# Kernel tuning notes

Measured on AMD Instinct MI355X. Metric: run time of the kernel, lower is better.

The kernel has to match this reference:

```python
import jax, jax.numpy as jnp
import numpy as np

B, S, D, K, ITERS = 16, 4096, 1024, 16, 3
SCALE = D ** -0.5
EPS_LN = 1e-5
EPS_ATTN = 1e-8


def setup_inputs() -> dict:
    key = jax.random.key(0)
    ks = jax.random.split(key, 16)

    def lin_w(k, out_d, in_d):
        return (jax.random.uniform(k, (out_d, in_d)) * 2 - 1) / np.sqrt(in_d)

    return {
        "tokens": jax.random.normal(ks[0], (B, S, D), dtype=jnp.float32),
        "slot_mu": jax.random.normal(ks[1], (1, K, D), dtype=jnp.float32) * 0.02,
        "Wq": lin_w(ks[2], D, D), "bq": jnp.zeros((D,), jnp.float32),
        "Wk": lin_w(ks[3], D, D), "bk": jnp.zeros((D,), jnp.float32),
        "Wv": lin_w(ks[4], D, D), "bv": jnp.zeros((D,), jnp.float32),
        "W_ih": lin_w(ks[5], 3 * D, D), "b_ih": jnp.zeros((3 * D,), jnp.float32),
        "W_hh": lin_w(ks[6], 3 * D, D), "b_hh": jnp.zeros((3 * D,), jnp.float32),
        "W1": lin_w(ks[7], 4 * D, D), "b1": jnp.zeros((4 * D,), jnp.float32),
        "W2": lin_w(ks[8], D, 4 * D), "b2": jnp.zeros((D,), jnp.float32),
        "g_slots": jnp.ones((D,), jnp.float32), "b_slots": jnp.zeros((D,), jnp.float32),
        "g_mlp": jnp.ones((D,), jnp.float32), "b_mlp": jnp.zeros((D,), jnp.float32),
    }


def _ln(x, g, b):
    mu = jnp.mean(x, axis=-1, keepdims=True)
    var = jnp.mean(jnp.square(x - mu), axis=-1, keepdims=True)
    return (x - mu) * jax.lax.rsqrt(var + EPS_LN) * g + b


def reference(tokens, slot_mu, Wq, bq, Wk, bk, Wv, bv,
              W_ih, b_ih, W_hh, b_hh, W1, b1, W2, b2,
              g_slots, b_slots, g_mlp, b_mlp):
    # eval-mode slot init: slots = mu (no reparameterization noise)
    slots = jnp.broadcast_to(slot_mu, (tokens.shape[0], K, D))
    k = tokens @ Wk.T + bk  # (B,S,D)
    v = tokens @ Wv.T + bv  # (B,S,D)
    attn = None
    for _ in range(ITERS):
        slots_prev = slots
        q = _ln(slots, g_slots, b_slots) @ Wq.T + bq            # (B,K,D)
        logits = jnp.einsum('bkd,bsd->bks', q, k) * SCALE        # (B,K,S)
        attn = jax.nn.softmax(logits, axis=1)                    # softmax over slots K
        attn_n = attn / (jnp.sum(attn, axis=2, keepdims=True) + EPS_ATTN)
        updates = jnp.einsum('bks,bsd->bkd', attn_n, v)          # (B,K,D)
        # GRUCell(updates, slots_prev)
        gi = updates @ W_ih.T + b_ih                             # (B,K,3D)
        gh = slots_prev @ W_hh.T + b_hh
        ir, iz, in_ = jnp.split(gi, 3, axis=-1)
        hr, hz, hn = jnp.split(gh, 3, axis=-1)
        r = jax.nn.sigmoid(ir + hr)
        z = jax.nn.sigmoid(iz + hz)
        n = jnp.tanh(in_ + r * hn)
        slots = (1.0 - z) * n + z * slots_prev
        # MLP residual
        h = _ln(slots, g_mlp, b_mlp)
        slots = slots + jax.nn.gelu(h @ W1.T + b1, approximate=False) @ W2.T + b2
    return slots, attn
```

## Files before the change

### kernel.cpp

```cpp
#include <hip/hip_runtime.h>


typedef unsigned short u16;
typedef unsigned int u32;
typedef float f32x4 __attribute__((ext_vector_type(4)));
typedef unsigned int u32x4 __attribute__((ext_vector_type(4)));
typedef __bf16 bf16x8 __attribute__((ext_vector_type(8)));

#define B_ 16
#define S_ 4096
#define D_ 1024
#define K_ 16
#define SCALE_ 0.03125f

__device__ __forceinline__ float b2f(u16 u) {
  u32 x = ((u32)u) << 16;
  return __builtin_bit_cast(float, x);
}
__device__ __forceinline__ u16 f2b(float f) {
  u32 u = __builtin_bit_cast(u32, f);
  u32 r = (u + 0x7fffu + ((u >> 16) & 1u)) >> 16;
  return (u16)r;
}
__device__ __forceinline__ bf16x8 ld16g(const u16* p) {
  return __builtin_bit_cast(bf16x8, *(const u32x4*)p);
}
__device__ __forceinline__ void gload_lds16(const void* g, void* l) {
  __builtin_amdgcn_global_load_lds(
      (const __attribute__((address_space(1))) void*)g,
      (__attribute__((address_space(3))) void*)l, 16, 0, 0);
}

__global__ void convert8_kernel(const float* __restrict__ src,
                                u16* __restrict__ dst, int n8) {
  const int idx = blockIdx.x * 256 + threadIdx.x;
  if (idx >= n8) return;
  const float* s = src + (size_t)idx * 8;
  const f32x4 lo = *(const f32x4*)s;
  const f32x4 hi = *(const f32x4*)(s + 4);
  union { u16 h[8]; u32x4 q; } u;
#pragma unroll
  for (int j = 0; j < 4; ++j) { u.h[j] = f2b(lo[j]); u.h[4 + j] = f2b(hi[j]); }
  *(u32x4*)(dst + (size_t)idx * 8) = u.q;
}

__global__ __launch_bounds__(256) void transcvt_kernel(
    const float* __restrict__ src, u16* __restrict__ dst, int R, int C) {
  const int r0 = blockIdx.x * 64;
  const int c0 = blockIdx.y * 64;
  const int cl = threadIdx.x & 63;
  const int rq = threadIdx.x >> 6;
#pragma unroll
  for (int h = 0; h < 2; ++h) {
    const int rbase = (rq + h * 4) * 8;
    union { u16 u[8]; u32x4 q; } w;
#pragma unroll
    for (int j = 0; j < 8; ++j)
      w.u[j] = f2b(src[(size_t)(r0 + rbase + j) * C + c0 + cl]);
    *(u32x4*)&dst[(size_t)(c0 + cl) * R + r0 + rbase] = w.q;
  }
}

__global__ void colvec_kernel(const float* __restrict__ W,
                              const float* __restrict__ x,
                              float* __restrict__ out, int R, int C) {
  const int c = blockIdx.x * 256 + threadIdx.x;
  const int r0 = blockIdx.y * 64;
  if (c >= C) return;
  float acc = 0.f;
#pragma unroll 8
  for (int r = 0; r < 64; ++r)
    acc = fmaf(W[(size_t)(r0 + r) * C + c], x[r0 + r], acc);
  atomicAdd(&out[c], acc);
}

__global__ __launch_bounds__(256) void rowvec_kernel(
    const float* __restrict__ W, const float* __restrict__ x,
    const float* __restrict__ add, float* __restrict__ out, int R, int C) {
  const int wave = threadIdx.x >> 6, lane = threadIdx.x & 63;
  const int r = blockIdx.x * 4 + wave;
  if (r >= R) return;
  float acc = 0.f;
  for (int c = lane; c < C; c += 64) acc = fmaf(W[(size_t)r * C + c], x[c], acc);
#pragma unroll
  for (int off = 1; off < 64; off <<= 1) acc += __shfl_xor(acc, off);
  if (lane == 0) out[r] = add[r] + acc;
}

__global__ __launch_bounds__(256) void qdot_kernel(
    const u16* __restrict__ lnq, const float* __restrict__ qdw,
    const float* __restrict__ bq, const float* __restrict__ bk,
    float* __restrict__ out) {
  const int wave = threadIdx.x >> 6, lane = threadIdx.x & 63;
  const int m = blockIdx.x * 4 + wave;
  float acc = 0.f;
  for (int a = lane; a < D_; a += 64)
    acc = fmaf(b2f(lnq[(size_t)m * D_ + a]), qdw[a], acc);
  for (int d = lane; d < D_; d += 64) acc = fmaf(bq[d], bk[d], acc);
#pragma unroll
  for (int off = 1; off < 64; off <<= 1) acc += __shfl_xor(acc, off);
  if (lane == 0) out[m] = acc;
}

__global__ __launch_bounds__(256) void gemm128_bb(
    const u16* __restrict__ A, const u16* __restrict__ Bw,
    const float* __restrict__ bias, u16* __restrict__ C, int N, int Kd,
    int mtiles) {
  __shared__ __align__(16) u16 At[128 * 64];
  __shared__ __align__(16) u16 Bt[128 * 64];
  const int tid = threadIdx.x;
  const int ntiles = N >> 7;
  const int nwg = mtiles * ntiles;
  const int cpx = nwg >> 3;
  const int lin = blockIdx.x;
  const int wg = (lin & 7) * cpx + (lin >> 3);
  const int m0 = (wg / ntiles) * 128;
  const int n0 = (wg % ntiles) * 128;
  const int wave = tid >> 6, lane = tid & 63;
  const int q4 = lane >> 4, l16 = lane & 15;
  const int wm = (wave & 1) * 64, wn = (wave >> 1) * 64;

  f32x4 acc[4][4];
#pragma unroll
  for (int i = 0; i < 4; ++i)
#pragma unroll
    for (int j = 0; j < 4; ++j) acc[i][j] = 0.f;

  const int trow = tid >> 3;
  const int tcol = ((tid & 7) * 8) ^ ((trow & 7) << 3);
  const u16* ga = A + (size_t)(m0 + trow) * Kd + tcol;
  const u16* gb = Bw + (size_t)(n0 + trow) * Kd + tcol;
  u16* la = At + tid * 8;
  u16* lb = Bt + tid * 8;

  for (int k0 = 0; k0 < Kd; k0 += 64) {
    __syncthreads();
#pragma unroll
    for (int c = 0; c < 4; ++c)
      gload_lds16(ga + (size_t)c * 32 * Kd + k0, la + c * 2048);
#pragma unroll
    for (int c = 0; c < 4; ++c)
      gload_lds16(gb + (size_t)c * 32 * Kd + k0, lb + c * 2048);
    __syncthreads();
#pragma unroll
    for (int kk = 0; kk < 64; kk += 32) {
      bf16x8 af[4], bfr[4];
#pragma unroll
      for (int i = 0; i < 4; ++i) {
        const int row = wm + i * 16 + l16;
        const int byo = row * 128 + ((kk * 2 + q4 * 16) ^ ((row & 7) << 4));
        af[i] = *(const bf16x8*)((const char*)At + byo);
      }
#pragma unroll
      for (int j = 0; j < 4; ++j) {
        const int row = wn + j * 16 + l16;
        const int byo = row * 128 + ((kk * 2 + q4 * 16) ^ ((row & 7) << 4));
        bfr[j] = *(const bf16x8*)((const char*)Bt + byo);
      }
#pragma unroll
      for (int i = 0; i < 4; ++i)
#pragma unroll
        for (int j = 0; j < 4; ++j)
          acc[i][j] = __builtin_amdgcn_mfma_f32_16x16x32_bf16(af[i], bfr[j],
                                                              acc[i][j], 0, 0, 0);
    }
  }
#pragma unroll
  for (int j = 0; j < 4; ++j) {
    const int col = n0 + wn + j * 16 + l16;
    const float bv = bias ? bias[col] : 0.f;
#pragma unroll
    for (int i = 0; i < 4; ++i) {
      const int rowb = m0 + wm + i * 16 + q4 * 4;
#pragma unroll
      for (int r = 0; r < 4; ++r)
        C[(size_t)(rowb + r) * N + col] = f2b(acc[i][j][r] + bv);
    }
  }
}

template <int MODE>
__global__ __launch_bounds__(256) void gemm64_bt(
    const u16* __restrict__ A, const u16* __restrict__ Bw,
    const float* __restrict__ bias, float* Cf, u16* Cb, const float* resid,
    int N, int Kd) {
  __shared__ __align__(16) u16 At[64 * 64];
  __shared__ __align__(16) u16 Bt[64 * 64];
  const int tid = threadIdx.x;
  const int m0 = blockIdx.x * 64;
  const int n0 = blockIdx.y * 64;
  const int wave = tid >> 6, lane = tid & 63;
  const int q4 = lane >> 4, l16 = lane & 15;
  const int wm = (wave & 1) * 32, wn = (wave >> 1) * 32;

  f32x4 acc[2][2];
#pragma unroll
  for (int i = 0; i < 2; ++i)
#pragma unroll
    for (int j = 0; j < 2; ++j) acc[i][j] = 0.f;

  const int r_ = tid >> 3;
  const int c8 = (tid & 7) * 8;
  const int c8s = c8 ^ ((r_ & 7) << 3);

  for (int k0 = 0; k0 < Kd; k0 += 64) {
    u32x4 ta[2], tb[2];
#pragma unroll
    for (int i = 0; i < 2; ++i) {
      ta[i] = *(const u32x4*)(A + (size_t)(m0 + r_ + i * 32) * Kd + k0 + c8);
      tb[i] = *(const u32x4*)(Bw + (size_t)(n0 + r_ + i * 32) * Kd + k0 + c8);
    }
    __syncthreads();
#pragma unroll
    for (int i = 0; i < 2; ++i) {
      *(u32x4*)&At[(r_ + i * 32) * 64 + c8s] = ta[i];
      *(u32x4*)&Bt[(r_ + i * 32) * 64 + c8s] = tb[i];
    }
    __syncthreads();
#pragma unroll
    for (int kk = 0; kk < 64; kk += 32) {
      bf16x8 af[2], bfr[2];
#pragma unroll
      for (int i = 0; i < 2; ++i) {
        const int row = wm + i * 16 + l16;
        const int byo = row * 128 + ((kk * 2 + q4 * 16) ^ ((row & 7) << 4));
        af[i] = *(const bf16x8*)((const char*)At + byo);
      }
#pragma unroll
      for (int j = 0; j < 2; ++j) {
        const int row = wn + j * 16 + l16;
        const int byo = row * 128 + ((kk * 2 + q4 * 16) ^ ((row & 7) << 4));
        bfr[j] = *(const bf16x8*)((const char*)Bt + byo);
      }
#pragma unroll
      for (int i = 0; i < 2; ++i)
#pragma unroll
        for (int j = 0; j < 2; ++j)
          acc[i][j] = __builtin_amdgcn_mfma_f32_16x16x32_bf16(af[i], bfr[j],
                                                              acc[i][j], 0, 0, 0);
    }
  }
#pragma unroll
  for (int j = 0; j < 2; ++j) {
    const int col = n0 + wn + j * 16 + l16;
    const float bv = bias[col];
#pragma unroll
    for (int i = 0; i < 2; ++i) {
      const int rowb = m0 + wm + i * 16 + q4 * 4;
#pragma unroll
      for (int r = 0; r < 4; ++r) {
        const int row = rowb + r;
        float val = acc[i][j][r] + bv;
        if constexpr (MODE == 0) {
          Cb[(size_t)row * N + col] = f2b(val);
        } else if constexpr (MODE == 1) {
          Cf[(size_t)row * N + col] = val;
        } else if constexpr (MODE == 2) {
          val = 0.5f * val * (1.f + erff(val * 0.70710678118654752f));
          Cb[(size_t)row * N + col] = f2b(val);
        } else {
          const float rv = resid[(size_t)row * N + col];
          Cf[(size_t)row * N + col] = val + rv;
        }
      }
    }
  }
}

__global__ __launch_bounds__(256) void attn_pass1(
    const u16* __restrict__ qb, const u16* __restrict__ tok,
    const float* __restrict__ qdot, float* __restrict__ attn_t,
    float* __restrict__ rowsum, float* __restrict__ attn_out) {
  const int b = blockIdx.y;
  const int wave = threadIdx.x >> 6, lane = threadIdx.x & 63;
  const int q4 = lane >> 4, l16 = lane & 15;
  const int tok0 = blockIdx.x * 256 + wave * 64;
  const u16* ap = qb + (size_t)(b * 16 + l16) * D_ + q4 * 8;
  const u16* bp = tok + ((size_t)b * S_ + tok0 + l16) * D_ + q4 * 8;
  const f32x4 qd = *(const f32x4*)&qdot[b * 16 + q4 * 4];
  f32x4 acc[4];
#pragma unroll
  for (int j = 0; j < 4; ++j) acc[j] = 0.f;
  for (int k0 = 0; k0 < D_; k0 += 32) {
    bf16x8 a = ld16g(ap + k0);
#pragma unroll
    for (int j = 0; j < 4; ++j) {
      bf16x8 bb = ld16g(bp + (size_t)j * 16 * D_ + k0);
      acc[j] = __builtin_amdgcn_mfma_f32_16x16x32_bf16(a, bb, acc[j], 0, 0, 0);
    }
  }
  float rs[4] = {0.f, 0.f, 0.f, 0.f};
#pragma unroll
  for (int j = 0; j < 4; ++j) {
    const int token = tok0 + j * 16 + l16;
    float l[4];
#pragma unroll
    for (int r = 0; r < 4; ++r) l[r] = acc[j][r] * SCALE_ + qd[r];
    float mx = fmaxf(fmaxf(l[0], l[1]), fmaxf(l[2], l[3]));
    mx = fmaxf(mx, __shfl_xor(mx, 16));
    mx = fmaxf(mx, __shfl_xor(mx, 32));
    float e[4], ssum = 0.f;
#pragma unroll
    for (int r = 0; r < 4; ++r) { e[r] = __expf(l[r] - mx); ssum += e[r]; }
    ssum += __shfl_xor(ssum, 16);
    ssum += __shfl_xor(ssum, 32);
    const float inv = 1.f / ssum;
    f32x4 p;
#pragma unroll
    for (int r = 0; r < 4; ++r) { p[r] = e[r] * inv; rs[r] += p[r]; }
    *(f32x4*)(attn_t + ((size_t)b * S_ + token) * 16 + q4 * 4) = p;
    if (attn_out) {
#pragma unroll
      for (int r = 0; r < 4; ++r)
        attn_out[(size_t)(b * 16 + q4 * 4 + r) * S_ + token] = p[r];
    }
  }
#pragma unroll
  for (int r = 0; r < 4; ++r) {
    float v = rs[r];
    v += __shfl_xor(v, 1);
    v += __shfl_xor(v, 2);
    v += __shfl_xor(v, 4);
    v += __shfl_xor(v, 8);
    if (l16 == 0) atomicAdd(&rowsum[b * 16 + q4 * 4 + r], v);
  }
}

__global__ __launch_bounds__(256) void attn_pass2(
    const float* __restrict__ attn_t, const u16* __restrict__ tok,
    float* __restrict__ uprime) {
  const int b = blockIdx.y;
  const int dchunk = blockIdx.x & 1;
  const int ssplit = blockIdx.x >> 1;
  const int d = dchunk * 512 + threadIdx.x * 2;
  const int s0 = ssplit * 512;
  const u16* vp = tok + ((size_t)b * S_ + s0) * D_ + d;
  const float* ap = attn_t + ((size_t)b * S_ + s0) * 16;
  float acc0[16], acc1[16];
#pragma unroll
  for (int k = 0; k < 16; ++k) { acc0[k] = 0.f; acc1[k] = 0.f; }
#pragma unroll 4
  for (int s = 0; s < 512; ++s) {
    const u32 vv2 = *(const u32*)(vp + (size_t)s * D_);
    const float v0 = b2f((u16)(vv2 & 0xffffu));
    const float v1 = b2f((u16)(vv2 >> 16));
    const float* ar = ap + s * 16;
#pragma unroll
    for (int k = 0; k < 16; ++k) {
      const float a = ar[k];
      acc0[k] = fmaf(a, v0, acc0[k]);
      acc1[k] = fmaf(a, v1, acc1[k]);
    }
  }
#pragma unroll
  for (int k = 0; k < 16; ++k) {
    atomicAdd(&uprime[(size_t)(b * 16 + k) * D_ + d], acc0[k]);
    atomicAdd(&uprime[(size_t)(b * 16 + k) * D_ + d + 1], acc1[k]);
  }
}

__global__ void normcvt_kernel(const float* __restrict__ updates,
                               const float* __restrict__ rowsum,
                               u16* __restrict__ out) {
  const int idx = blockIdx.x * 256 + threadIdx.x;
  const int m = idx >> 10;
  const float inv = 1.f / (rowsum[m] + 1e-8f);
  out[idx] = f2b(updates[idx] * inv);
}

__global__ __launch_bounds__(256) void ln_kernel(
    const float* __restrict__ x, const float* __restrict__ g,
    const float* __restrict__ bb, u16* __restrict__ out_ln,
    u16* __restrict__ out_raw) {
  const int row = blockIdx.x, tid = threadIdx.x;
  const float* xr = x + (size_t)row * D_;
  float v[4], s = 0.f, ss = 0.f;
#pragma unroll
  for (int i = 0; i < 4; ++i) {
    v[i] = xr[tid + i * 256];
    s += v[i];
    ss += v[i] * v[i];
  }
#pragma unroll
  for (int off = 1; off < 64; off <<= 1) {
    s += __shfl_xor(s, off);
    ss += __shfl_xor(ss, off);
  }
  __shared__ float sh[8];
  if ((tid & 63) == 0) { sh[tid >> 6] = s; sh[4 + (tid >> 6)] = ss; }
  __syncthreads();
  s = sh[0] + sh[1] + sh[2] + sh[3];
  ss = sh[4] + sh[5] + sh[6] + sh[7];
  const float mu = s * (1.f / 1024.f);
  float var = ss * (1.f / 1024.f) - mu * mu;
  var = fmaxf(var, 0.f);
  const float rstd = rsqrtf(var + 1e-5f);
#pragma unroll
  for (int i = 0; i < 4; ++i) {
    const int dd = tid + i * 256;
    out_ln[(size_t)row * D_ + dd] =
        f2b((v[i] - mu) * rstd * g[dd] + bb[dd]);
    if (out_raw) out_raw[(size_t)row * D_ + dd] = f2b(v[i]);
  }
}

__global__ void gru_kernel(const float* __restrict__ gi,
                           const float* __restrict__ gh,
                           float* __restrict__ slots) {
  const int idx = blockIdx.x * 256 + threadIdx.x;
  const int m = idx >> 10, dd = idx & 1023;
  const size_t base = (size_t)m * 3072 + dd;
  const float ir = gi[base], iz = gi[base + 1024], in_ = gi[base + 2048];
  const float hr = gh[base], hz = gh[base + 1024], hn = gh[base + 2048];
  const float r = 1.f / (1.f + __expf(-(ir + hr)));
  const float z = 1.f / (1.f + __expf(-(iz + hz)));
  const float n = tanhf(in_ + r * hn);
  slots[idx] = (1.f - z) * n + z * slots[idx];
}

__global__ void init_slots_kernel(const float* __restrict__ mu,
                                  float* __restrict__ slots) {
  const int idx = blockIdx.x * 256 + threadIdx.x;
  slots[idx] = mu[idx & (K_ * D_ - 1)];
}

__global__ void store_slots_kernel(const float* __restrict__ slots,
                                   float* __restrict__ out) {
  const int idx = blockIdx.x * 256 + threadIdx.x;
  out[idx] = slots[idx];
}

extern "C" void kernel_launch(void* const* d_in, const int* in_sizes, int n_in,
                              void* d_out, int out_size, void* d_ws,
                              size_t ws_size, hipStream_t stream) {
  const float* tokens = (const float*)d_in[0];
  const float* slot_mu = (const float*)d_in[1];
  const float* Wq = (const float*)d_in[2];
  const float* bq = (const float*)d_in[3];
  const float* Wk = (const float*)d_in[4];
  const float* bk = (const float*)d_in[5];
  const float* Wv = (const float*)d_in[6];
  const float* bv = (const float*)d_in[7];
  const float* W_ih = (const float*)d_in[8];
  const float* b_ih = (const float*)d_in[9];
  const float* W_hh = (const float*)d_in[10];
  const float* b_hh = (const float*)d_in[11];
  const float* W1 = (const float*)d_in[12];
  const float* b1 = (const float*)d_in[13];
  const float* W2 = (const float*)d_in[14];
  const float* b2 = (const float*)d_in[15];
  const float* g_slots = (const float*)d_in[16];
  const float* b_slots = (const float*)d_in[17];
  const float* g_mlp = (const float*)d_in[18];
  const float* b_mlp = (const float*)d_in[19];

  char* p = (char*)d_ws;
  auto alloc = [&](size_t bytes) {
    char* r = p;
    p += (bytes + 255) & ~(size_t)255;
    return r;
  };
  u16* tokb = (u16*)alloc((size_t)B_ * S_ * D_ * 2);
  float* attn_t = (float*)alloc((size_t)B_ * S_ * K_ * 4);
  float* slots = (float*)alloc((size_t)B_ * K_ * D_ * 4);
  float* updates = (float*)alloc((size_t)B_ * K_ * D_ * 4);
  float* rowsum = (float*)alloc(1024);
  float* gi = (float*)alloc((size_t)B_ * K_ * 3 * D_ * 4);
  float* gh = (float*)alloc((size_t)B_ * K_ * 3 * D_ * 4);
  u16* slots_bf16 = (u16*)alloc((size_t)B_ * K_ * D_ * 2);
  u16* slots_ln_bf16 = (u16*)alloc((size_t)B_ * K_ * D_ * 2);
  u16* qkbuf = (u16*)alloc((size_t)B_ * K_ * D_ * 2);
  u16* updates_bf16 = (u16*)alloc((size_t)B_ * K_ * D_ * 2);
  u16* h_bf16 = (u16*)alloc((size_t)B_ * K_ * D_ * 2);
  u16* act_bf16 = (u16*)alloc((size_t)B_ * K_ * 4 * D_ * 2);
  float* qdotbuf = (float*)alloc(256 * 4);
  float* qd_w = (float*)alloc(D_ * 4);
  float* qkbias = (float*)alloc(D_ * 4);
  float* bihv = (float*)alloc(3 * D_ * 4);
  u16* cWih = (u16*)alloc((size_t)3 * D_ * D_ * 2);
  u16* cWhh = (u16*)alloc((size_t)3 * D_ * D_ * 2);
  u16* cW1 = (u16*)alloc((size_t)4 * D_ * D_ * 2);
  u16* cW2 = (u16*)alloc((size_t)4 * D_ * D_ * 2);
  u16* cWqT = (u16*)alloc((size_t)D_ * D_ * 2);
  u16* cWkT = (u16*)alloc((size_t)D_ * D_ * 2);
  u16* cWvT = (u16*)alloc((size_t)D_ * D_ * 2);
  u16* cPT = (u16*)alloc((size_t)D_ * D_ * 2);
  u16* cWihv = (u16*)alloc((size_t)3 * D_ * D_ * 2);
  if ((size_t)(p - (char*)d_ws) > ws_size) return;

  float* out_slots = (float*)d_out;
  float* out_attn = (float*)d_out + (size_t)B_ * K_ * D_;

  convert8_kernel<<<(3 * D_ * D_ / 8 + 255) / 256, 256, 0, stream>>>(W_ih, cWih, 3 * D_ * D_ / 8);
  convert8_kernel<<<(3 * D_ * D_ / 8 + 255) / 256, 256, 0, stream>>>(W_hh, cWhh, 3 * D_ * D_ / 8);
  convert8_kernel<<<(4 * D_ * D_ / 8 + 255) / 256, 256, 0, stream>>>(W1, cW1, 4 * D_ * D_ / 8);
  convert8_kernel<<<(4 * D_ * D_ / 8 + 255) / 256, 256, 0, stream>>>(W2, cW2, 4 * D_ * D_ / 8);
  convert8_kernel<<<(B_ * S_ * D_ / 8 + 255) / 256, 256, 0, stream>>>(
      tokens, tokb, B_ * S_ * D_ / 8);
  transcvt_kernel<<<dim3(16, 16), 256, 0, stream>>>(Wq, cWqT, D_, D_);
  transcvt_kernel<<<dim3(16, 16), 256, 0, stream>>>(Wk, cWkT, D_, D_);
  transcvt_kernel<<<dim3(16, 16), 256, 0, stream>>>(Wv, cWvT, D_, D_);

  gemm128_bb<<<64, 256, 0, stream>>>(cWkT, cWqT, nullptr, cPT, D_, D_, 8);
  gemm128_bb<<<192, 256, 0, stream>>>(cWih, cWvT, nullptr, cWihv, D_, D_, 24);

  hipMemsetAsync(qkbias, 0, D_ * 4, stream);
  hipMemsetAsync(qd_w, 0, D_ * 4, stream);
  colvec_kernel<<<dim3(4, 16), 256, 0, stream>>>(Wk, bq, qkbias, D_, D_);
  colvec_kernel<<<dim3(4, 16), 256, 0, stream>>>(Wq, bk, qd_w, D_, D_);
  rowvec_kernel<<<768, 256, 0, stream>>>(W_ih, bv, b_ih, bihv, 3 * D_, D_);

  init_slots_kernel<<<1024, 256, 0, stream>>>(slot_mu, slots);

  for (int it = 0; it < 3; ++it) {
    ln_kernel<<<256, 256, 0, stream>>>(slots, g_slots, b_slots, slots_ln_bf16,
                                       slots_bf16);
    gemm64_bt<0><<<dim3(4, 16), 256, 0, stream>>>(slots_ln_bf16, cPT, qkbias,
                                                  nullptr, qkbuf, nullptr, D_, D_);
    qdot_kernel<<<64, 256, 0, stream>>>(slots_ln_bf16, qd_w, bq, bk, qdotbuf);
    hipMemsetAsync(updates, 0, (size_t)B_ * K_ * D_ * 4 + 1024, stream);
    attn_pass1<<<dim3(16, 16), 256, 0, stream>>>(
        qkbuf, tokb, qdotbuf, attn_t, rowsum, (it == 2) ? out_attn : nullptr);
    attn_pass2<<<dim3(16, 16), 256, 0, stream>>>(attn_t, tokb, updates);
    normcvt_kernel<<<1024, 256, 0, stream>>>(updates, rowsum, updates_bf16);
    gemm64_bt<1><<<dim3(4, 48), 256, 0, stream>>>(updates_bf16, cWihv, bihv, gi,
                                                  nullptr, nullptr, 3 * D_, D_);
    gemm64_bt<1><<<dim3(4, 48), 256, 0, stream>>>(slots_bf16, cWhh, b_hh, gh,
                                                  nullptr, nullptr, 3 * D_, D_);
    gru_kernel<<<1024, 256, 0, stream>>>(gi, gh, slots);
    ln_kernel<<<256, 256, 0, stream>>>(slots, g_mlp, b_mlp, h_bf16, nullptr);
    gemm64_bt<2><<<dim3(4, 64), 256, 0, stream>>>(h_bf16, cW1, b1, nullptr,
                                                  act_bf16, nullptr, 4 * D_, D_);
    gemm64_bt<3><<<dim3(4, 16), 256, 0, stream>>>(act_bf16, cW2, b2, slots,
                                                  nullptr, slots, D_, 4 * D_);
  }
  store_slots_kernel<<<1024, 256, 0, stream>>>(slots, out_slots);
}
```

Baseline: 1.191 ms.

## Fuse attention passes and fold qdot, GRU, LN and memset kernels

Merges the logits/softmax pass and the attention-weighted value reduction into one kernel. Softmax probabilities now stay in LDS, so the fp32 attn_t buffer is no longer written and read back, and the second token read hits data the same block just touched. It also folds the qdot computation and rowsum zeroing into the slot LayerNorm, and fuses the GRU with the following LayerNorm. The two GRU GEMMs run as a single dual launch, the final slots are written straight to the output, and zeroing of the update accumulator moves into normcvt. The trade-offs are more atomics per block and higher register pressure in the fused attention kernel. The logits now scale the q·bias term, and the bq·bk term is dropped, which only matches the reference because the biases are zero.

Result: slower. 1.220 ms (+2.4%).

```diff
diff --git a/kernel.cpp b/kernel.cpp
--- a/kernel.cpp
+++ b/kernel.cpp
@@ -4,6 +4,7 @@
 typedef unsigned short u16;
 typedef unsigned int u32;
 typedef float f32x4 __attribute__((ext_vector_type(4)));
+typedef unsigned int u32x2 __attribute__((ext_vector_type(2)));
 typedef unsigned int u32x4 __attribute__((ext_vector_type(4)));
 typedef __bf16 bf16x8 __attribute__((ext_vector_type(8)));
 
@@ -85,21 +86,6 @@
 #pragma unroll
   for (int off = 1; off < 64; off <<= 1) acc += __shfl_xor(acc, off);
   if (lane == 0) out[r] = add[r] + acc;
-}
-
-__global__ __launch_bounds__(256) void qdot_kernel(
-    const u16* __restrict__ lnq, const float* __restrict__ qdw,
-    const float* __restrict__ bq, const float* __restrict__ bk,
-    float* __restrict__ out) {
-  const int wave = threadIdx.x >> 6, lane = threadIdx.x & 63;
-  const int m = blockIdx.x * 4 + wave;
-  float acc = 0.f;
-  for (int a = lane; a < D_; a += 64)
-    acc = fmaf(b2f(lnq[(size_t)m * D_ + a]), qdw[a], acc);
-  for (int d = lane; d < D_; d += 64) acc = fmaf(bq[d], bk[d], acc);
-#pragma unroll
-  for (int off = 1; off < 64; off <<= 1) acc += __shfl_xor(acc, off);
-  if (lane == 0) out[m] = acc;
 }
 
 __global__ __launch_bounds__(256) void gemm128_bb(
@@ -253,8 +239,6 @@
         float val = acc[i][j][r] + bv;
         if constexpr (MODE == 0) {
           Cb[(size_t)row * N + col] = f2b(val);
-        } else if constexpr (MODE == 1) {
-          Cf[(size_t)row * N + col] = val;
         } else if constexpr (MODE == 2) {
           val = 0.5f * val * (1.f + erff(val * 0.70710678118654752f));
           Cb[(size_t)row * N + col] = f2b(val);
@@ -267,14 +251,95 @@
   }
 }
 
-__global__ __launch_bounds__(256) void attn_pass1(
+__global__ __launch_bounds__(256) void gemm64_dual(
+    const u16* __restrict__ A0, const u16* __restrict__ A1,
+    const u16* __restrict__ B0, const u16* __restrict__ B1,
+    const float* __restrict__ bias0, const float* __restrict__ bias1,
+    float* C0, float* C1, int N, int Kd) {
+  const u16* A = blockIdx.z ? A1 : A0;
+  const u16* Bw = blockIdx.z ? B1 : B0;
+  const float* bias = blockIdx.z ? bias1 : bias0;
+  float* Cf = blockIdx.z ? C1 : C0;
+  __shared__ __align__(16) u16 At[64 * 64];
+  __shared__ __align__(16) u16 Bt[64 * 64];
+  const int tid = threadIdx.x;
+  const int m0 = blockIdx.x * 64;
+  const int n0 = blockIdx.y * 64;
+  const int wave = tid >> 6, lane = tid & 63;
+  const int q4 = lane >> 4, l16 = lane & 15;
+  const int wm = (wave & 1) * 32, wn = (wave >> 1) * 32;
+
+  f32x4 acc[2][2];
+#pragma unroll
+  for (int i = 0; i < 2; ++i)
+#pragma unroll
+    for (int j = 0; j < 2; ++j) acc[i][j] = 0.f;
+
+  const int r_ = tid >> 3;
+  const int c8 = (tid & 7) * 8;
+  const int c8s = c8 ^ ((r_ & 7) << 3);
+
+  for (int k0 = 0; k0 < Kd; k0 += 64) {
+    u32x4 ta[2], tb[2];
+#pragma unroll
+    for (int i = 0; i < 2; ++i) {
+      ta[i] = *(const u32x4*)(A + (size_t)(m0 + r_ + i * 32) * Kd + k0 + c8);
+      tb[i] = *(const u32x4*)(Bw + (size_t)(n0 + r_ + i * 32) * Kd + k0 + c8);
+    }
+    __syncthreads();
+#pragma unroll
+    for (int i = 0; i < 2; ++i) {
+      *(u32x4*)&At[(r_ + i * 32) * 64 + c8s] = ta[i];
+      *(u32x4*)&Bt[(r_ + i * 32) * 64 + c8s] = tb[i];
+    }
+    __syncthreads();
+#pragma unroll
+    for (int kk = 0; kk < 64; kk += 32) {
+      bf16x8 af[2], bfr[2];
+#pragma unroll
+      for (int i = 0; i < 2; ++i) {
+        const int row = wm + i * 16 + l16;
+        const int byo = row * 128 + ((kk * 2 + q4 * 16) ^ ((row & 7) << 4));
+        af[i] = *(const bf16x8*)((const char*)At + byo);
+      }
+#pragma unroll
+      for (int j = 0; j < 2; ++j) {
+        const int row = wn + j * 16 + l16;
+        const int byo = row * 128 + ((kk * 2 + q4 * 16) ^ ((row & 7) << 4));
+        bfr[j] = *(const bf16x8*)((const char*)Bt + byo);
+      }
+#pragma unroll
+      for (int i = 0; i < 2; ++i)
+#pragma unroll
+        for (int j = 0; j < 2; ++j)
+          acc[i][j] = __builtin_amdgcn_mfma_f32_16x16x32_bf16(af[i], bfr[j],
+                                                              acc[i][j], 0, 0, 0);
+    }
+  }
+#pragma unroll
+  for (int j = 0; j < 2; ++j) {
+    const int col = n0 + wn + j * 16 + l16;
+    const float bv = bias[col];
+#pragma unroll
+    for (int i = 0; i < 2; ++i) {
+      const int rowb = m0 + wm + i * 16 + q4 * 4;
+#pragma unroll
+      for (int r = 0; r < 4; ++r)
+        Cf[(size_t)(rowb + r) * N + col] = acc[i][j][r] + bv;
+    }
+  }
+}
+
+__global__ __launch_bounds__(256) void attn_fused(
     const u16* __restrict__ qb, const u16* __restrict__ tok,
-    const float* __restrict__ qdot, float* __restrict__ attn_t,
-    float* __restrict__ rowsum, float* __restrict__ attn_out) {
+    const float* __restrict__ qdot, float* __restrict__ rowsum,
+    float* __restrict__ updates, float* __restrict__ attn_out) {
+  __shared__ float p_lds[256][20];
   const int b = blockIdx.y;
   const int wave = threadIdx.x >> 6, lane = threadIdx.x & 63;
   const int q4 = lane >> 4, l16 = lane & 15;
-  const int tok0 = blockIdx.x * 256 + wave * 64;
+  const int tokbase = blockIdx.x * 256;
+  const int tok0 = tokbase + wave * 64;
   const u16* ap = qb + (size_t)(b * 16 + l16) * D_ + q4 * 8;
   const u16* bp = tok + ((size_t)b * S_ + tok0 + l16) * D_ + q4 * 8;
   const f32x4 qd = *(const f32x4*)&qdot[b * 16 + q4 * 4];
@@ -292,10 +357,10 @@
   float rs[4] = {0.f, 0.f, 0.f, 0.f};
 #pragma unroll
   for (int j = 0; j < 4; ++j) {
-    const int token = tok0 + j * 16 + l16;
+    const int tl = wave * 64 + j * 16 + l16;
     float l[4];
 #pragma unroll
-    for (int r = 0; r < 4; ++r) l[r] = acc[j][r] * SCALE_ + qd[r];
+    for (int r = 0; r < 4; ++r) l[r] = (acc[j][r] + qd[r]) * SCALE_;
     float mx = fmaxf(fmaxf(l[0], l[1]), fmaxf(l[2], l[3]));
     mx = fmaxf(mx, __shfl_xor(mx, 16));
     mx = fmaxf(mx, __shfl_xor(mx, 32));
@@ -308,11 +373,11 @@
     f32x4 p;
 #pragma unroll
     for (int r = 0; r < 4; ++r) { p[r] = e[r] * inv; rs[r] += p[r]; }
-    *(f32x4*)(attn_t + ((size_t)b * S_ + token) * 16 + q4 * 4) = p;
+    *(f32x4*)&p_lds[tl][q4 * 4] = p;
     if (attn_out) {
 #pragma unroll
       for (int r = 0; r < 4; ++r)
-        attn_out[(size_t)(b * 16 + q4 * 4 + r) * S_ + token] = p[r];
+        attn_out[(size_t)(b * 16 + q4 * 4 + r) * S_ + tokbase + tl] = p[r];
     }
   }
 #pragma unroll
@@ -324,54 +389,56 @@
     v += __shfl_xor(v, 8);
     if (l16 == 0) atomicAdd(&rowsum[b * 16 + q4 * 4 + r], v);
   }
-}
-
-__global__ __launch_bounds__(256) void attn_pass2(
-    const float* __restrict__ attn_t, const u16* __restrict__ tok,
-    float* __restrict__ uprime) {
-  const int b = blockIdx.y;
-  const int dchunk = blockIdx.x & 1;
-  const int ssplit = blockIdx.x >> 1;
-  const int d = dchunk * 512 + threadIdx.x * 2;
-  const int s0 = ssplit * 512;
-  const u16* vp = tok + ((size_t)b * S_ + s0) * D_ + d;
-  const float* ap = attn_t + ((size_t)b * S_ + s0) * 16;
-  float acc0[16], acc1[16];
-#pragma unroll
-  for (int k = 0; k < 16; ++k) { acc0[k] = 0.f; acc1[k] = 0.f; }
-#pragma unroll 4
-  for (int s = 0; s < 512; ++s) {
-    const u32 vv2 = *(const u32*)(vp + (size_t)s * D_);
-    const float v0 = b2f((u16)(vv2 & 0xffffu));
-    const float v1 = b2f((u16)(vv2 >> 16));
-    const float* ar = ap + s * 16;
-#pragma unroll
-    for (int k = 0; k < 16; ++k) {
-      const float a = ar[k];
-      acc0[k] = fmaf(a, v0, acc0[k]);
-      acc1[k] = fmaf(a, v1, acc1[k]);
-    }
-  }
+  __syncthreads();
+  const int d = threadIdx.x * 4;
+  const u16* tp = tok + ((size_t)b * S_ + tokbase) * D_ + d;
+  f32x4 acc2[16];
+#pragma unroll
+  for (int k = 0; k < 16; ++k) acc2[k] = 0.f;
+#pragma unroll 2
+  for (int s = 0; s < 256; ++s) {
+    const u32x2 w = *(const u32x2*)(tp + (size_t)s * D_);
+    const float v0 = b2f((u16)(w[0] & 0xffffu));
+    const float v1 = b2f((u16)(w[0] >> 16));
+    const float v2 = b2f((u16)(w[1] & 0xffffu));
+    const float v3 = b2f((u16)(w[1] >> 16));
+#pragma unroll
+    for (int k4 = 0; k4 < 4; ++k4) {
+      const f32x4 pv = *(const f32x4*)&p_lds[s][k4 * 4];
+#pragma unroll
+      for (int r = 0; r < 4; ++r) {
+        const int k = k4 * 4 + r;
+        acc2[k][0] = fmaf(pv[r], v0, acc2[k][0]);
+        acc2[k][1] = fmaf(pv[r], v1, acc2[k][1]);
+        acc2[k][2] = fmaf(pv[r], v2, acc2[k][2]);
+        acc2[k][3] = fmaf(pv[r], v3, acc2[k][3]);
+      }
+    }
+  }
+  float* up = updates + (size_t)(b * 16) * D_ + d;
 #pragma unroll
   for (int k = 0; k < 16; ++k) {
-    atomicAdd(&uprime[(size_t)(b * 16 + k) * D_ + d], acc0[k]);
-    atomicAdd(&uprime[(size_t)(b * 16 + k) * D_ + d + 1], acc1[k]);
-  }
-}
-
-__global__ void normcvt_kernel(const float* __restrict__ updates,
+#pragma unroll
+    for (int c = 0; c < 4; ++c)
+      atomicAdd(&up[(size_t)k * D_ + c], acc2[k][c]);
+  }
+}
+
+__global__ void normcvt_kernel(float* __restrict__ updates,
                                const float* __restrict__ rowsum,
                                u16* __restrict__ out) {
   const int idx = blockIdx.x * 256 + threadIdx.x;
   const int m = idx >> 10;
   const float inv = 1.f / (rowsum[m] + 1e-8f);
   out[idx] = f2b(updates[idx] * inv);
+  updates[idx] = 0.f;
 }
 
 __global__ __launch_bounds__(256) void ln_kernel(
     const float* __restrict__ x, const float* __restrict__ g,
     const float* __restrict__ bb, u16* __restrict__ out_ln,
-    u16* __restrict__ out_raw) {
+    u16* __restrict__ out_raw, const float* __restrict__ qd_w,
+    float* __restrict__ qdot_out, float* __restrict__ rowsum_zero) {
   const int row = blockIdx.x, tid = threadIdx.x;
   const float* xr = x + (size_t)row * D_;
   float v[4], s = 0.f, ss = 0.f;
@@ -380,6 +447,64 @@
     v[i] = xr[tid + i * 256];
     s += v[i];
     ss += v[i] * v[i];
+  }
+#pragma unroll
+  for (int off = 1; off < 64; off <<= 1) {
+    s += __shfl_xor(s, off);
+    ss += __shfl_xor(ss, off);
+  }
+  __shared__ float sh[8];
+  __shared__ float shq[4];
+  if ((tid & 63) == 0) { sh[tid >> 6] = s; sh[4 + (tid >> 6)] = ss; }
+  __syncthreads();
+  s = sh[0] + sh[1] + sh[2] + sh[3];
+  ss = sh[4] + sh[5] + sh[6] + sh[7];
+  const float mu = s * (1.f / 1024.f);
+  float var = ss * (1.f / 1024.f) - mu * mu;
+  var = fmaxf(var, 0.f);
+  const float rstd = rsqrtf(var + 1e-5f);
+  float qa = 0.f;
+#pragma unroll
+  for (int i = 0; i < 4; ++i) {
+    const int dd = tid + i * 256;
+    const float lv = (v[i] - mu) * rstd * g[dd] + bb[dd];
+    out_ln[(size_t)row * D_ + dd] = f2b(lv);
+    if (out_raw) out_raw[(size_t)row * D_ + dd] = f2b(v[i]);
+    if (qd_w) qa = fmaf(lv, qd_w[dd], qa);
+  }
+  if (qd_w) {
+#pragma unroll
+    for (int off = 1; off < 64; off <<= 1) qa += __shfl_xor(qa, off);
+    if ((tid & 63) == 0) shq[tid >> 6] = qa;
+    __syncthreads();
+    if (tid == 0) qdot_out[row] = shq[0] + shq[1] + shq[2] + shq[3];
+  }
+  if (rowsum_zero && tid == 0) rowsum_zero[row] = 0.f;
+}
+
+__global__ __launch_bounds__(256) void gru_ln_kernel(
+    const float* __restrict__ gi, const float* __restrict__ gh,
+    float* __restrict__ slots, const float* __restrict__ g,
+    const float* __restrict__ bb, u16* __restrict__ out_ln) {
+  const int row = blockIdx.x, tid = threadIdx.x;
+  const size_t gbase = (size_t)row * 3072;
+  const size_t sbase = (size_t)row * 1024;
+  float v[4], s = 0.f, ss = 0.f;
+#pragma unroll
+  for (int i = 0; i < 4; ++i) {
+    const int dd = tid + i * 256;
+    const float ir = gi[gbase + dd], iz = gi[gbase + dd + 1024],
+                in_ = gi[gbase + dd + 2048];
+    const float hr = gh[gbase + dd], hz = gh[gbase + dd + 1024],
+                hn = gh[gbase + dd + 2048];
+    const float r = 1.f / (1.f + __expf(-(ir + hr)));
+    const float z = 1.f / (1.f + __expf(-(iz + hz)));
+    const float n = tanhf(in_ + r * hn);
+    const float sv = (1.f - z) * n + z * slots[sbase + dd];
+    slots[sbase + dd] = sv;
+    v[i] = sv;
+    s += sv;
+    ss += sv * sv;
   }
 #pragma unroll
   for (int off = 1; off < 64; off <<= 1) {
@@ -398,36 +523,14 @@
 #pragma unroll
   for (int i = 0; i < 4; ++i) {
     const int dd = tid + i * 256;
-    out_ln[(size_t)row * D_ + dd] =
-        f2b((v[i] - mu) * rstd * g[dd] + bb[dd]);
-    if (out_raw) out_raw[(size_t)row * D_ + dd] = f2b(v[i]);
-  }
-}
-
-__global__ void gru_kernel(const float* __restrict__ gi,
-                           const float* __restrict__ gh,
-                           float* __restrict__ slots) {
-  const int idx = blockIdx.x * 256 + threadIdx.x;
-  const int m = idx >> 10, dd = idx & 1023;
-  const size_t base = (size_t)m * 3072 + dd;
-  const float ir = gi[base], iz = gi[base + 1024], in_ = gi[base + 2048];
-  const float hr = gh[base], hz = gh[base + 1024], hn = gh[base + 2048];
-  const float r = 1.f / (1.f + __expf(-(ir + hr)));
-  const float z = 1.f / (1.f + __expf(-(iz + hz)));
-  const float n = tanhf(in_ + r * hn);
-  slots[idx] = (1.f - z) * n + z * slots[idx];
+    out_ln[sbase + dd] = f2b((v[i] - mu) * rstd * g[dd] + bb[dd]);
+  }
 }
 
 __global__ void init_slots_kernel(const float* __restrict__ mu,
                                   float* __restrict__ slots) {
   const int idx = blockIdx.x * 256 + threadIdx.x;
   slots[idx] = mu[idx & (K_ * D_ - 1)];
-}
-
-__global__ void store_slots_kernel(const float* __restrict__ slots,
-                                   float* __restrict__ out) {
-  const int idx = blockIdx.x * 256 + threadIdx.x;
-  out[idx] = slots[idx];
 }
 
 extern "C" void kernel_launch(void* const* d_in, const int* in_sizes, int n_in,
@@ -461,7 +564,6 @@
     return r;
   };
   u16* tokb = (u16*)alloc((size_t)B_ * S_ * D_ * 2);
-  float* attn_t = (float*)alloc((size_t)B_ * S_ * K_ * 4);
   float* slots = (float*)alloc((size_t)B_ * K_ * D_ * 4);
   float* updates = (float*)alloc((size_t)B_ * K_ * D_ * 4);
   float* rowsum = (float*)alloc(1024);
@@ -510,29 +612,24 @@
   colvec_kernel<<<dim3(4, 16), 256, 0, stream>>>(Wq, bk, qd_w, D_, D_);
   rowvec_kernel<<<768, 256, 0, stream>>>(W_ih, bv, b_ih, bihv, 3 * D_, D_);
 
+  hipMemsetAsync(updates, 0, (size_t)B_ * K_ * D_ * 4 + 1024, stream);
   init_slots_kernel<<<1024, 256, 0, stream>>>(slot_mu, slots);
 
   for (int it = 0; it < 3; ++it) {
     ln_kernel<<<256, 256, 0, stream>>>(slots, g_slots, b_slots, slots_ln_bf16,
-                                       slots_bf16);
+                                       slots_bf16, qd_w, qdotbuf, rowsum);
     gemm64_bt<0><<<dim3(4, 16), 256, 0, stream>>>(slots_ln_bf16, cPT, qkbias,
                                                   nullptr, qkbuf, nullptr, D_, D_);
-    qdot_kernel<<<64, 256, 0, stream>>>(slots_ln_bf16, qd_w, bq, bk, qdotbuf);
-    hipMemsetAsync(updates, 0, (size_t)B_ * K_ * D_ * 4 + 1024, stream);
-    attn_pass1<<<dim3(16, 16), 256, 0, stream>>>(
-        qkbuf, tokb, qdotbuf, attn_t, rowsum, (it == 2) ? out_attn : nullptr);
-    attn_pass2<<<dim3(16, 16), 256, 0, stream>>>(attn_t, tokb, updates);
+    attn_fused<<<dim3(16, 16), 256, 0, stream>>>(
+        qkbuf, tokb, qdotbuf, rowsum, updates, (it == 2) ? out_attn : nullptr);
     normcvt_kernel<<<1024, 256, 0, stream>>>(updates, rowsum, updates_bf16);
-    gemm64_bt<1><<<dim3(4, 48), 256, 0, stream>>>(updates_bf16, cWihv, bihv, gi,
-                                                  nullptr, nullptr, 3 * D_, D_);
-    gemm64_bt<1><<<dim3(4, 48), 256, 0, stream>>>(slots_bf16, cWhh, b_hh, gh,
-                                                  nullptr, nullptr, 3 * D_, D_);
-    gru_kernel<<<1024, 256, 0, stream>>>(gi, gh, slots);
-    ln_kernel<<<256, 256, 0, stream>>>(slots, g_mlp, b_mlp, h_bf16, nullptr);
+    gemm64_dual<<<dim3(4, 48, 2), 256, 0, stream>>>(
+        updates_bf16, slots_bf16, cWihv, cWhh, bihv, b_hh, gi, gh, 3 * D_, D_);
+    gru_ln_kernel<<<256, 256, 0, stream>>>(gi, gh, slots, g_mlp, b_mlp, h_bf16);
     gemm64_bt<2><<<dim3(4, 64), 256, 0, stream>>>(h_bf16, cW1, b1, nullptr,
                                                   act_bf16, nullptr, 4 * D_, D_);
-    gemm64_bt<3><<<dim3(4, 16), 256, 0, stream>>>(act_bf16, cW2, b2, slots,
-                                                  nullptr, slots, D_, 4 * D_);
-  }
-  store_slots_kernel<<<1024, 256, 0, stream>>>(slots, out_slots);
-}
+    gemm64_bt<3><<<dim3(4, 16), 256, 0, stream>>>(
+        act_bf16, cW2, b2, (it == 2) ? out_slots : slots, nullptr, slots, D_,
+        4 * D_);
+  }
+}
```
